# Performance work log

Measured on AMD Instinct MI355X. Metric: run time of the kernel, lower is better.

## Reference

```python
import jax, jax.numpy as jnp
import numpy as np
import math

B, S, K, H, NH = 4, 1024, 512, 1024, 16
HD = H // NH  # 64


def _split_heads(x):
    # [B, L, H] -> [B, NH, L, HD]
    b, l, _ = x.shape
    return x.reshape(b, l, NH, HD).transpose(0, 2, 1, 3)


def setup_inputs() -> dict:
    key = jax.random.key(0)
    ks = jax.random.split(key, 16)
    scale = 1.0 / math.sqrt(H)
    d = {
        'hidden_states': jax.random.normal(ks[0], (B, S, H), jnp.float32),
        'encoder_hidden_states': jax.random.normal(ks[1], (B, K, H), jnp.float32),
        'attention_mask': jnp.zeros((B, 1, 1, S), jnp.float32),
        'encoder_attention_mask': jnp.zeros((B, 1, 1, K), jnp.float32),
    }
    names = ['q', 'k', 'v', 'kq', 'kk', 'kv']
    for i, n in enumerate(names):
        d[f'W{n}'] = jax.random.normal(ks[2 + i], (H, H), jnp.float32) * scale
        d[f'b{n}'] = jnp.zeros((H,), jnp.float32)
    return d


def reference(hidden_states, encoder_hidden_states, attention_mask, encoder_attention_mask,
              Wq, bq, Wk, bk, Wv, bv, Wkq, bkq, Wkk, bkk, Wkv, bkv):
    inv = 1.0 / math.sqrt(HD)
    # self branch
    q = _split_heads(hidden_states @ Wq + bq)            # [B,NH,S,HD]
    k = _split_heads(hidden_states @ Wk + bk)
    v = _split_heads(hidden_states @ Wv + bv)
    scores = jnp.einsum('bhsd,bhtd->bhst', q, k) * inv + attention_mask
    probs = jax.nn.softmax(scores, axis=-1)              # [B,NH,S,S]
    ctx = jnp.einsum('bhst,bhtd->bhsd', probs, v)
    # knowledge branch
    kq = _split_heads(hidden_states @ Wkq + bkq)          # [B,NH,S,HD]
    kk = _split_heads(encoder_hidden_states @ Wkk + bkk)  # [B,NH,K,HD]
    kv = _split_heads(encoder_hidden_states @ Wkv + bkv)
    kscores = jnp.einsum('bhsd,bhtd->bhst', kq, kk) * inv + encoder_attention_mask
    kprobs = jax.nn.softmax(kscores, axis=-1)            # [B,NH,S,K]
    kctx = jnp.einsum('bhst,bhtd->bhsd', kprobs, kv)
    # merge heads and average branches
    out = (ctx + kctx) * 0.5                             # [B,NH,S,HD]
    out = out.transpose(0, 2, 1, 3).reshape(B, S, H)
    return out
```

## Files before the change

### kernel.cpp

```cpp
#include <hip/hip_runtime.h>

#define BATCH 4
#define SEQ   1024
#define KENC  512
#define HDIM  1024
#define NHEAD 16
#define HD    64
#define LOG2E 1.44269504088896340736f

typedef __attribute__((ext_vector_type(8))) short bf16x8;
typedef __attribute__((ext_vector_type(4))) float f32x4;
typedef __attribute__((ext_vector_type(16))) float f32x16;
typedef __attribute__((ext_vector_type(4))) float f4v;
typedef __attribute__((ext_vector_type(4))) short s4v;

__device__ __forceinline__ short f2bf(float f) {
  unsigned u = __float_as_uint(f);
  u += 0x7fffu + ((u >> 16) & 1u);
  return (short)(u >> 16);
}

__device__ __forceinline__ void gload_lds16(const void* g, void* l) {
  __builtin_amdgcn_global_load_lds(
      (const __attribute__((address_space(1))) void*)g,
      (__attribute__((address_space(3))) void*)l, 16, 0, 0);
}

__device__ __forceinline__ float tmax16(const f32x16& v) {
  float a0 = fmaxf(v[0], v[1]),   a1 = fmaxf(v[2], v[3]);
  float a2 = fmaxf(v[4], v[5]),   a3 = fmaxf(v[6], v[7]);
  float a4 = fmaxf(v[8], v[9]),   a5 = fmaxf(v[10], v[11]);
  float a6 = fmaxf(v[12], v[13]), a7 = fmaxf(v[14], v[15]);
  float b0 = fmaxf(a0, a1), b1 = fmaxf(a2, a3);
  float b2 = fmaxf(a4, a5), b3 = fmaxf(a6, a7);
  return fmaxf(fmaxf(b0, b1), fmaxf(b2, b3));
}
__device__ __forceinline__ float tsum16(const f32x16& v) {
  float a0 = v[0] + v[1],   a1 = v[2] + v[3];
  float a2 = v[4] + v[5],   a3 = v[6] + v[7];
  float a4 = v[8] + v[9],   a5 = v[10] + v[11];
  float a6 = v[12] + v[13], a7 = v[14] + v[15];
  float b0 = a0 + a1, b1 = a2 + a3, b2 = a4 + a5, b3 = a6 + a7;
  return (b0 + b1) + (b2 + b3);
}

#define MF(A, B, C) __builtin_amdgcn_mfma_f32_16x16x32_bf16((A), (B), (C), 0, 0, 0)

struct PrepArgs { const float* W[6]; };

__global__ __launch_bounds__(256) void prep(PrepArgs a, short* __restrict__ wt,
                                            const float* __restrict__ hid,
                                            short* __restrict__ hbf, int n4h,
                                            const float* __restrict__ enc,
                                            short* __restrict__ ebf, int n4e) {
  __shared__ float t[32][33];
  int blk = blockIdx.x;
  if (blk < 6144) {
    int j = blk >> 10;
    int r = blk & 1023;
    int cb = (r & 31) * 32, rb = (r >> 5) * 32;
    const float* W = a.W[j];
    short* dst = wt + (size_t)j * (HDIM * HDIM);
    int tx = threadIdx.x & 31, ty = threadIdx.x >> 5;
#pragma unroll
    for (int rr = 0; rr < 4; ++rr)
      t[ty + rr * 8][tx] = W[(size_t)(rb + ty + rr * 8) * HDIM + cb + tx];
    __syncthreads();
#pragma unroll
    for (int rr = 0; rr < 4; ++rr)
      dst[(size_t)(cb + ty + rr * 8) * HDIM + rb + tx] = f2bf(t[tx][ty + rr * 8]);
  } else {
    int i = (blk - 6144) * 256 + threadIdx.x;
    const float* s;
    short* d;
    int j;
    if (i < n4h) { s = hid; d = hbf; j = i; }
    else { j = i - n4h; if (j >= n4e) return; s = enc; d = ebf; }
    f4v v = ((const f4v*)s)[j];
    s4v o;
#pragma unroll
    for (int k = 0; k < 4; ++k) o[k] = f2bf(v[k]);
    ((s4v*)d)[j] = o;
  }
}

struct ProjArgs {
  const short* X[6];
  const short* Wt[6];
  const float* bias[6];
  short* out[6];
  int M[6];
  int tshift[6];
  int mode[6];
  float scale[6];
};

__global__ __launch_bounds__(256) void proj_gemm(ProjArgs a) {
  int job = blockIdx.z;
  int M = a.M[job];
  int by = blockIdx.y;
  if (by * 128 >= M) return;
  int bx = blockIdx.x;
  const short* X = a.X[job];
  const short* W = a.Wt[job];

  __shared__ __align__(16) char Lds[65536];

  int tid = threadIdx.x, lane = tid & 63, wave = tid >> 6;
  int wr = wave >> 1, wc = wave & 1;
  int l15 = lane & 15, g4 = lane >> 4;

  f32x4 acc[4][4];
#pragma unroll
  for (int m = 0; m < 4; ++m)
#pragma unroll
    for (int n = 0; n < 4; ++n)
#pragma unroll
      for (int r = 0; r < 4; ++r) acc[m][n][r] = 0.0f;

  int arow = by * 128, brow = bx * 128;
  const int crow = lane >> 2;
  const int sgrp = (lane & 3) ^ ((lane >> 2) & 3) ^ (lane >> 4);
  const int rsw = (lane & 3) ^ (l15 >> 2);

  const char* Xb = (const char*)X;
  const char* Wb = (const char*)W;
  const size_t sac0 = ((size_t)(arow + 32 * wave + crow) * HDIM + sgrp * 8) * 2;
  const size_t sac1 = sac0 + (size_t)16 * HDIM * 2;
  const size_t sbc0 = ((size_t)(brow + 32 * wave + crow) * HDIM + sgrp * 8) * 2;
  const size_t sbc1 = sbc0 + (size_t)16 * HDIM * 2;
  const int ldA0 = wave * 2048, ldA1 = ldA0 + 1024;
  const int ldB0 = 8192 + ldA0, ldB1 = ldB0 + 1024;

  const int aoff = wr * 4096 + l15 * 64 + ((g4 ^ rsw) << 4);
  const int boff = 8192 + wc * 4096 + l15 * 64 + ((g4 ^ rsw) << 4);

#define STG_A(SBO, SKT)                                                  \
  do {                                                                   \
    gload_lds16(Xb + sac0 + (size_t)(SKT) * 64, Lds + (SBO) + ldA0);     \
    gload_lds16(Xb + sac1 + (size_t)(SKT) * 64, Lds + (SBO) + ldA1);     \
  } while (0)
#define STG_B(SBO, SKT)                                                  \
  do {                                                                   \
    gload_lds16(Wb + sbc0 + (size_t)(SKT) * 64, Lds + (SBO) + ldB0);     \
    gload_lds16(Wb + sbc1 + (size_t)(SKT) * 64, Lds + (SBO) + ldB1);     \
  } while (0)

  STG_A(0, 0);     STG_B(0, 0);
  STG_A(16384, 1); STG_B(16384, 1);
  STG_A(32768, 2); STG_B(32768, 2);
  asm volatile("s_waitcnt vmcnt(4)" ::: "memory");
  __builtin_amdgcn_s_barrier();
  asm volatile("" ::: "memory");

  bf16x8 xa0, xa1, xb0, xb1, xb2, xb3;
  bf16x8 ya0, ya1, yb0, yb1, yb2, yb3;

  xa0 = *(const bf16x8*)(Lds + 0 * 1024 + aoff);
  xa1 = *(const bf16x8*)(Lds + 1 * 1024 + aoff);
  xb0 = *(const bf16x8*)(Lds + 0 * 1024 + boff);
  xb1 = *(const bf16x8*)(Lds + 1 * 1024 + boff);
  xb2 = *(const bf16x8*)(Lds + 2 * 1024 + boff);
  xb3 = *(const bf16x8*)(Lds + 3 * 1024 + boff);

#define GSTEP_I(BO, BON, CA0, CA1, CB0, CB1, CB2, CB3, NA0, NA1, NB0, NB1,    \
                NB2, NB3, DO_STG, SBO, SKT, DO_NEXT, VMASM, DO_BAR)           \
  do {                                                                        \
    bf16x8 q2 = *(const bf16x8*)(Lds + (BO) + 2 * 1024 + aoff);               \
    bf16x8 q3 = *(const bf16x8*)(Lds + (BO) + 3 * 1024 + aoff);               \
    if (DO_STG) STG_A(SBO, SKT);                                              \
    __builtin_amdgcn_s_setprio(1);                                            \
    acc[0][0] = MF(CA0, CB0, acc[0][0]);                                      \
    acc[0][1] = MF(CA0, CB1, acc[0][1]);                                      \
    acc[0][2] = MF(CA0, CB2, acc[0][2]);                                      \
    acc[0][3] = MF(CA0, CB3, acc[0][3]);                                      \
    acc[1][0] = MF(CA1, CB0, acc[1][0]);                                      \
    acc[1][1] = MF(CA1, CB1, acc[1][1]);                                      \
    acc[1][2] = MF(CA1, CB2, acc[1][2]);                                      \
    acc[1][3] = MF(CA1, CB3, acc[1][3]);                                      \
    __builtin_amdgcn_s_setprio(0);                                            \
    if (DO_NEXT) {                                                            \
      NA0 = *(const bf16x8*)(Lds + (BON) + 0 * 1024 + aoff);                  \
      NA1 = *(const bf16x8*)(Lds + (BON) + 1 * 1024 + aoff);                  \
      NB0 = *(const bf16x8*)(Lds + (BON) + 0 * 1024 + boff);                  \
      NB1 = *(const bf16x8*)(Lds + (BON) + 1 * 1024 + boff);                  \
      NB2 = *(const bf16x8*)(Lds + (BON) + 2 * 1024 + boff);                  \
      NB3 = *(const bf16x8*)(Lds + (BON) + 3 * 1024 + boff);                  \
    }                                                                         \
    if (DO_STG) STG_B(SBO, SKT);                                              \
    __builtin_amdgcn_s_setprio(1);                                            \
    acc[2][0] = MF(q2, CB0, acc[2][0]);                                       \
    acc[2][1] = MF(q2, CB1, acc[2][1]);                                       \
    acc[2][2] = MF(q2, CB2, acc[2][2]);                                       \
    acc[2][3] = MF(q2, CB3, acc[2][3]);                                       \
    acc[3][0] = MF(q3, CB0, acc[3][0]);                                       \
    acc[3][1] = MF(q3, CB1, acc[3][1]);                                       \
    acc[3][2] = MF(q3, CB2, acc[3][2]);                                       \
    acc[3][3] = MF(q3, CB3, acc[3][3]);                                       \
    __builtin_amdgcn_s_setprio(0);                                            \
    asm volatile(VMASM ::: "memory");                                         \
    if (DO_BAR) {                                                             \
      __builtin_amdgcn_s_barrier();                                           \
      asm volatile("" ::: "memory");                                          \
    }                                                                         \
  } while (0)
#define GSTEP(...) GSTEP_I(__VA_ARGS__)

#define XSET xa0, xa1, xb0, xb1, xb2, xb3
#define YSET ya0, ya1, yb0, yb1, yb2, yb3

#pragma unroll 1
  for (int it = 0; it < 7; ++it) {
    int t0 = it * 4;
    GSTEP(0,     16384, XSET, YSET, 1, 49152, t0 + 3, 1, "s_waitcnt vmcnt(4)", 1);
    GSTEP(16384, 32768, YSET, XSET, 1, 0,     t0 + 4, 1, "s_waitcnt vmcnt(4)", 1);
    GSTEP(32768, 49152, XSET, YSET, 1, 16384, t0 + 5, 1, "s_waitcnt vmcnt(4)", 1);
    GSTEP(49152, 0,     YSET, XSET, 1, 32768, t0 + 6, 1, "s_waitcnt vmcnt(4)", 1);
  }
  GSTEP(0,     16384, XSET, YSET, 1, 49152, 31, 1, "s_waitcnt vmcnt(4)", 1);
  GSTEP(16384, 32768, YSET, XSET, 0, 0, 0,      1, "s_waitcnt vmcnt(0)", 1);
  GSTEP(32768, 49152, XSET, YSET, 0, 0, 0,      1, "s_nop 0", 1);
  GSTEP(49152, 0,     YSET, XSET, 0, 0, 0,      0, "s_nop 0", 0);

#undef GSTEP
#undef GSTEP_I
#undef XSET
#undef YSET
#undef STG_A
#undef STG_B

  const float* bias = a.bias[job];
  short* out = a.out[job];
  int tshift = a.tshift[job], tmask = (1 << tshift) - 1, mode = a.mode[job];
  float scl = a.scale[job];
#pragma unroll
  for (int m = 0; m < 4; ++m) {
    int rowb = arow + wr * 64 + m * 16 + (g4 << 2);
#pragma unroll
    for (int n = 0; n < 4; ++n) {
      int col = brow + wc * 64 + n * 16 + l15;
      float bv = bias[col];
      int head = col >> 6, d = col & 63;
#pragma unroll
      for (int r = 0; r < 4; ++r) {
        int row = rowb + r;
        int bb = row >> tshift, tk = row & tmask;
        float val = (acc[m][n][r] + bv) * scl;
        size_t idx;
        if (mode == 0)
          idx = ((((size_t)bb * NHEAD + head) << tshift) + tk) * 64 + d;
        else
          idx = ((((size_t)bb * NHEAD + head) * 64 + d) << tshift) + tk;
        out[idx] = f2bf(val);
      }
    }
  }
}

__global__ __launch_bounds__(128, 2) void attn32(
    const short* __restrict__ qall, const short* __restrict__ kall,
    const short* __restrict__ vTall, const short* __restrict__ kqall,
    const short* __restrict__ kkall, const short* __restrict__ kvTall,
    const float* __restrict__ amask, const float* __restrict__ emask,
    float* __restrict__ out) {
  __shared__ char KT[2][8192];
  __shared__ char VT[2][8192];
  __shared__ float red[2][32];

  int lid = blockIdx.x;
  int id = (lid & 7) * 128 + (lid >> 3);
  int bh = id >> 4, qb = id & 15;
  int b = bh >> 4, h = bh & 15;
  int lane = threadIdx.x & 63, wave = threadIdx.x >> 6;
  int l31 = lane & 31, hi = lane >> 5, x7 = l31 & 7;
  int qrow0 = qb * 64 + wave * 32;

  bf16x8 qcur[4];
  {
    const short* qp = qall + ((size_t)bh * SEQ + qrow0 + l31) * 64;
#pragma unroll
    for (int i = 0; i < 4; ++i)
      qcur[i] = *(const bf16x8*)(qp + i * 16 + hi * 8);
  }

  const char* kb0 = (const char*)(kall + (size_t)bh * SEQ * 64);
  const char* vb0 = (const char*)(vTall + (size_t)bh * 64 * SEQ);
  const char* kb1 = (const char*)(kkall + (size_t)bh * KENC * 64);
  const char* vb1 = (const char*)(kvTall + (size_t)bh * 64 * KENC);
  const float* mpc = amask + (size_t)b * SEQ;

  auto STAGE = [&](int pb, const char* kb, const char* vb, size_t vrowb, int kt) {
    int t0 = threadIdx.x;
#pragma unroll
    for (int c = 0; c < 4; ++c) {
      int idx = c * 128 + t0;
      int row = idx >> 3, phys = idx & 7;
      int lg = phys ^ (row & 7);
      gload_lds16(kb + ((size_t)(kt * 64 + row)) * 128 + lg * 16,
                  KT[pb] + idx * 16);
      gload_lds16(vb + (size_t)row * vrowb + (size_t)kt * 128 + lg * 16,
                  VT[pb] + idx * 16);
    }
  };

  STAGE(0, kb0, vb0, SEQ * 2, 0);

  f32x16 ctx0, ctx1, c10, c11;
#pragma unroll
  for (int r = 0; r < 16; ++r) { ctx0[r] = 0.f; ctx1[r] = 0.f; c10[r] = 0.f; c11[r] = 0.f; }
  float mr = -1e30f, lr = 0.f;

#pragma unroll 1
  for (int t = 0; t < 24; ++t) {
    int p = t & 1;
    __syncthreads();
    if (t < 23) {
      int tn = t + 1;
      if (tn >= 16) STAGE(p ^ 1, kb1, vb1, KENC * 2, tn - 16);
      else          STAGE(p ^ 1, kb0, vb0, SEQ * 2, tn);
    }
    if (t == 16) {
      if (!hi) red[wave][l31] = lr;
      asm volatile("s_waitcnt lgkmcnt(0)" ::: "memory");
#pragma unroll
      for (int r2 = 0; r2 < 4; ++r2) {
        f4v lv = *(const f4v*)(&red[wave][r2 * 8 + 4 * hi]);
#pragma unroll
        for (int j2 = 0; j2 < 4; ++j2) {
          float li = __builtin_amdgcn_rcpf(lv[j2]);
          int r = r2 * 4 + j2;
          c10[r] = ctx0[r] * li;  ctx0[r] = 0.f;
          c11[r] = ctx1[r] * li;  ctx1[r] = 0.f;
        }
      }
      mr = -1e30f; lr = 0.f;
      const short* kqp = kqall + ((size_t)bh * SEQ + qrow0 + l31) * 64;
#pragma unroll
      for (int i = 0; i < 4; ++i)
        qcur[i] = *(const bf16x8*)(kqp + i * 16 + hi * 8);
      mpc = emask + (size_t)b * KENC;
    }
    int kt = (t >= 16) ? t - 16 : t;
    const char* Kp = KT[p];
    const char* Vp = VT[p];

    f32x16 s0, s1;
#pragma unroll
    for (int r = 0; r < 16; ++r) { s0[r] = 0.f; s1[r] = 0.f; }
    __builtin_amdgcn_s_setprio(1);
#pragma unroll
    for (int i = 0; i < 4; ++i) {
      bf16x8 kf = *(const bf16x8*)(Kp + (l31)*128 + (((2 * i + hi) ^ x7) << 4));
      s0 = __builtin_amdgcn_mfma_f32_32x32x16_bf16(kf, qcur[i], s0, 0, 0, 0);
    }
#pragma unroll
    for (int i = 0; i < 4; ++i) {
      bf16x8 kf = *(const bf16x8*)(Kp + (32 + l31) * 128 + (((2 * i + hi) ^ x7) << 4));
      s1 = __builtin_amdgcn_mfma_f32_32x32x16_bf16(kf, qcur[i], s1, 0, 0, 0);
    }
    __builtin_amdgcn_s_setprio(0);

    const float* mp = mpc + kt * 64;
#pragma unroll
    for (int r2 = 0; r2 < 4; ++r2) {
      f4v ma = *(const f4v*)(mp + r2 * 8 + 4 * hi);
      f4v mb = *(const f4v*)(mp + 32 + r2 * 8 + 4 * hi);
#pragma unroll
      for (int j2 = 0; j2 < 4; ++j2) {
        s0[r2 * 4 + j2] = fmaf(ma[j2], LOG2E, s0[r2 * 4 + j2]);
        s1[r2 * 4 + j2] = fmaf(mb[j2], LOG2E, s1[r2 * 4 + j2]);
      }
    }

    float mx = fmaxf(tmax16(s0), tmax16(s1));
    mx = fmaxf(mx, __int_as_float(__shfl_xor(__float_as_int(mx), 32)));

    if (!__all(mx <= mr + 12.f)) {
      float mn = fmaxf(mr, mx);
      float scl = __builtin_amdgcn_exp2f(mr - mn);
      mr = mn; lr *= scl;
      if (!hi) red[wave][l31] = scl;
      asm volatile("s_waitcnt lgkmcnt(0)" ::: "memory");
#pragma unroll
      for (int r2 = 0; r2 < 4; ++r2) {
        f4v sv = *(const f4v*)(&red[wave][r2 * 8 + 4 * hi]);
#pragma unroll
        for (int j2 = 0; j2 < 4; ++j2) {
          ctx0[r2 * 4 + j2] *= sv[j2];
          ctx1[r2 * 4 + j2] *= sv[j2];
        }
      }
    }

#pragma unroll
    for (int r = 0; r < 16; ++r) s0[r] = __builtin_amdgcn_exp2f(s0[r] - mr);
#pragma unroll
    for (int r = 0; r < 16; ++r) s1[r] = __builtin_amdgcn_exp2f(s1[r] - mr);
    float rs = tsum16(s0) + tsum16(s1);
    rs += __int_as_float(__shfl_xor(__float_as_int(rs), 32));
    lr += rs;

#pragma unroll
    for (int s = 0; s < 2; ++s) {
      const f32x16& sv = s ? s1 : s0;
      unsigned W[8];
#pragma unroll
      for (int r2 = 0; r2 < 4; ++r2) {
        asm("v_cvt_pk_bf16_f32 %0, %1, %2"
            : "=v"(W[r2 * 2]) : "v"(sv[r2 * 4 + 0]), "v"(sv[r2 * 4 + 1]));
        asm("v_cvt_pk_bf16_f32 %0, %1, %2"
            : "=v"(W[r2 * 2 + 1]) : "v"(sv[r2 * 4 + 2]), "v"(sv[r2 * 4 + 3]));
      }
#pragma unroll
      for (int jr = 0; jr < 2; ++jr) {
        unsigned sendA = hi ? W[(2 * jr) * 2]     : W[(2 * jr + 1) * 2];
        unsigned sendB = hi ? W[(2 * jr) * 2 + 1] : W[(2 * jr + 1) * 2 + 1];
        unsigned rA = (unsigned)__shfl_xor((int)sendA, 32);
        unsigned rB = (unsigned)__shfl_xor((int)sendB, 32);
        union { unsigned u[4]; bf16x8 v; } pa;
        if (!hi) { pa.u[0] = W[2 * jr * 2]; pa.u[1] = W[2 * jr * 2 + 1];
                   pa.u[2] = rA;            pa.u[3] = rB; }
        else     { pa.u[0] = rA;            pa.u[1] = rB;
                   pa.u[2] = W[(2 * jr + 1) * 2]; pa.u[3] = W[(2 * jr + 1) * 2 + 1]; }
        int j = s * 2 + jr;
        __builtin_amdgcn_s_setprio(1);
        bf16x8 vf0 = *(const bf16x8*)(Vp + (l31)*128 + (((2 * j + hi) ^ x7) << 4));
        ctx0 = __builtin_amdgcn_mfma_f32_32x32x16_bf16(pa.v, vf0, ctx0, 0, 0, 0);
        bf16x8 vf1 = *(const bf16x8*)(Vp + (32 + l31) * 128 + (((2 * j + hi) ^ x7) << 4));
        ctx1 = __builtin_amdgcn_mfma_f32_32x32x16_bf16(pa.v, vf1, ctx1, 0, 0, 0);
        __builtin_amdgcn_s_setprio(0);
      }
    }
  }

  if (!hi) red[wave][l31] = lr;
  asm volatile("s_waitcnt lgkmcnt(0)" ::: "memory");
  float* op = out + ((size_t)b * SEQ) * HDIM + h * 64 + l31;
#pragma unroll
  for (int r2 = 0; r2 < 4; ++r2) {
    f4v lv = *(const f4v*)(&red[wave][r2 * 8 + 4 * hi]);
#pragma unroll
    for (int j2 = 0; j2 < 4; ++j2) {
      float li = __builtin_amdgcn_rcpf(lv[j2]);
      int s = qrow0 + r2 * 8 + 4 * hi + j2;
      int r = r2 * 4 + j2;
      op[(size_t)s * HDIM]      = 0.5f * (c10[r] + ctx0[r] * li);
      op[(size_t)s * HDIM + 32] = 0.5f * (c11[r] + ctx1[r] * li);
    }
  }
}

extern "C" void kernel_launch(void* const* d_in, const int* in_sizes, int n_in,
                              void* d_out, int out_size, void* d_ws, size_t ws_size,
                              hipStream_t stream) {
  const float* hid = (const float*)d_in[0];
  const float* enc = (const float*)d_in[1];
  const float* amask = (const float*)d_in[2];
  const float* emask = (const float*)d_in[3];

  char* ws = (char*)d_ws;
  short* hbf = (short*)(ws);
  short* ebf = (short*)(ws + (8u << 20));
  short* wt = (short*)(ws + (12u << 20));
  short* qo = (short*)(ws + (24u << 20));
  short* ko = (short*)(ws + (32u << 20));
  short* vT = (short*)(ws + (40u << 20));
  short* kqo = (short*)(ws + (48u << 20));
  short* kko = (short*)(ws + (56u << 20));
  short* kvT = (short*)(ws + (60u << 20));

  PrepArgs wa;
  for (int j = 0; j < 6; ++j) wa.W[j] = (const float*)d_in[4 + 2 * j];
  prep<<<12288, 256, 0, stream>>>(wa, wt, hid, hbf, (BATCH * SEQ * HDIM) / 4,
                                  enc, ebf, (BATCH * KENC * HDIM) / 4);

  ProjArgs pa;
  const short* Xs[6] = {hbf, hbf, hbf, hbf, ebf, ebf};
  short* outs[6] = {qo, ko, vT, kqo, kko, kvT};
  const int Ms[6] = {4096, 4096, 4096, 4096, 2048, 2048};
  const int tsh[6] = {10, 10, 10, 10, 9, 9};
  const int md[6] = {0, 0, 1, 0, 0, 1};
  const float qscale = 0.125f * LOG2E;
  const float scl[6] = {qscale, 1.f, 1.f, qscale, 1.f, 1.f};
  for (int j = 0; j < 6; ++j) {
    pa.X[j] = Xs[j];
    pa.Wt[j] = wt + (size_t)j * (HDIM * HDIM);
    pa.bias[j] = (const float*)d_in[5 + 2 * j];
    pa.out[j] = outs[j];
    pa.M[j] = Ms[j];
    pa.tshift[j] = tsh[j];
    pa.mode[j] = md[j];
    pa.scale[j] = scl[j];
  }
  proj_gemm<<<dim3(8, 32, 6), 256, 0, stream>>>(pa);

  attn32<<<1024, 128, 0, stream>>>(qo, ko, vT, kqo, kko, kvT, amask, emask,
                                   (float*)d_out);
}
```

Baseline: 139.7 us.

## Rewrite projection GEMM with 256x256 tiles, 8 waves, and compact job grid

Replaces the 128x128-tile, 4-wave projection GEMM with a 256x256-tile, 8-wave kernel. It uses 128KB of LDS, 64-wide K slices with double buffering, and a new XOR swizzle. The 3D grid with early-exit blocks becomes a flat 320-block grid that maps block ids directly to job and tile, so no empty blocks launch. Larger tiles raise operand reuse and cut global traffic. The cost is fewer blocks (320 on a GPU with 256 CUs, leaving an unbalanced tail), more barriers per phase, and higher register pressure from 128 accumulators per thread.

Measured after the change: 162.9 us. +16.5%, slower.

```diff
diff --git a/kernel.cpp b/kernel.cpp
--- a/kernel.cpp
+++ b/kernel.cpp
@@ -89,156 +89,141 @@
   const short* Wt[6];
   const float* bias[6];
   short* out[6];
-  int M[6];
   int tshift[6];
   int mode[6];
   float scale[6];
 };
 
-__global__ __launch_bounds__(256) void proj_gemm(ProjArgs a) {
-  int job = blockIdx.z;
-  int M = a.M[job];
-  int by = blockIdx.y;
-  if (by * 128 >= M) return;
-  int bx = blockIdx.x;
-  const short* X = a.X[job];
-  const short* W = a.Wt[job];
-
-  __shared__ __align__(16) char Lds[65536];
+__global__ __launch_bounds__(512) void proj_gemm8(ProjArgs a) {
+  int id = blockIdx.x;
+  int job, bm, bn;
+  if (id < 256) { job = id >> 6; int r = id & 63; bm = r >> 2; bn = r & 3; }
+  else { int u = id - 256; job = 4 + (u >> 5); int r = u & 31; bm = r >> 2; bn = r & 3; }
+
+  const char* Xb = (const char*)a.X[job];
+  const char* Wb = (const char*)a.Wt[job];
+
+  __shared__ __align__(16) char Lds[131072];
 
   int tid = threadIdx.x, lane = tid & 63, wave = tid >> 6;
-  int wr = wave >> 1, wc = wave & 1;
-  int l15 = lane & 15, g4 = lane >> 4;
-
-  f32x4 acc[4][4];
-#pragma unroll
-  for (int m = 0; m < 4; ++m)
+  int wr = wave >> 2, wc = wave & 3;
+  int l15 = lane & 15, g4 = lane >> 4, x7 = l15 & 7;
+
+  f32x4 acc[8][4];
+#pragma unroll
+  for (int m = 0; m < 8; ++m)
 #pragma unroll
     for (int n = 0; n < 4; ++n)
 #pragma unroll
       for (int r = 0; r < 4; ++r) acc[m][n][r] = 0.0f;
 
-  int arow = by * 128, brow = bx * 128;
-  const int crow = lane >> 2;
-  const int sgrp = (lane & 3) ^ ((lane >> 2) & 3) ^ (lane >> 4);
-  const int rsw = (lane & 3) ^ (l15 >> 2);
-
-  const char* Xb = (const char*)X;
-  const char* Wb = (const char*)W;
-  const size_t sac0 = ((size_t)(arow + 32 * wave + crow) * HDIM + sgrp * 8) * 2;
-  const size_t sac1 = sac0 + (size_t)16 * HDIM * 2;
-  const size_t sbc0 = ((size_t)(brow + 32 * wave + crow) * HDIM + sgrp * 8) * 2;
-  const size_t sbc1 = sbc0 + (size_t)16 * HDIM * 2;
-  const int ldA0 = wave * 2048, ldA1 = ldA0 + 1024;
-  const int ldB0 = 8192 + ldA0, ldB1 = ldB0 + 1024;
-
-  const int aoff = wr * 4096 + l15 * 64 + ((g4 ^ rsw) << 4);
-  const int boff = 8192 + wc * 4096 + l15 * 64 + ((g4 ^ rsw) << 4);
-
-#define STG_A(SBO, SKT)                                                  \
-  do {                                                                   \
-    gload_lds16(Xb + sac0 + (size_t)(SKT) * 64, Lds + (SBO) + ldA0);     \
-    gload_lds16(Xb + sac1 + (size_t)(SKT) * 64, Lds + (SBO) + ldA1);     \
+  const int scol = (((lane & 7) ^ (lane >> 3)) << 4);
+  const size_t sA = ((size_t)(bm * 256 + wave * 8 + (lane >> 3))) * 2048 + scol;
+  const size_t sB = ((size_t)(bn * 256 + wave * 8 + (lane >> 3))) * 2048 + scol;
+  const int woff = wave * 1024;
+
+#define STG_T(SRC, SOFF, DB, KT)                                              \
+  do {                                                                        \
+    gload_lds16((SRC) + (SOFF) + (size_t)(KT) * 128, Lds + (DB) + woff);      \
+    gload_lds16((SRC) + (SOFF) + 131072 + (size_t)(KT) * 128,                 \
+                Lds + (DB) + 8192 + woff);                                    \
+    gload_lds16((SRC) + (SOFF) + 262144 + (size_t)(KT) * 128,                 \
+                Lds + (DB) + 16384 + woff);                                   \
+    gload_lds16((SRC) + (SOFF) + 393216 + (size_t)(KT) * 128,                 \
+                Lds + (DB) + 24576 + woff);                                   \
   } while (0)
-#define STG_B(SBO, SKT)                                                  \
-  do {                                                                   \
-    gload_lds16(Wb + sbc0 + (size_t)(SKT) * 64, Lds + (SBO) + ldB0);     \
-    gload_lds16(Wb + sbc1 + (size_t)(SKT) * 64, Lds + (SBO) + ldB1);     \
+#define STG_AB(SLOT, KT)                                                      \
+  do {                                                                        \
+    STG_T(Xb, sA, (SLOT) * 32768, KT);                                        \
+    STG_T(Wb, sB, 65536 + (SLOT) * 32768, KT);                                \
   } while (0)
 
-  STG_A(0, 0);     STG_B(0, 0);
-  STG_A(16384, 1); STG_B(16384, 1);
-  STG_A(32768, 2); STG_B(32768, 2);
-  asm volatile("s_waitcnt vmcnt(4)" ::: "memory");
-  __builtin_amdgcn_s_barrier();
-  asm volatile("" ::: "memory");
-
-  bf16x8 xa0, xa1, xb0, xb1, xb2, xb3;
-  bf16x8 ya0, ya1, yb0, yb1, yb2, yb3;
-
-  xa0 = *(const bf16x8*)(Lds + 0 * 1024 + aoff);
-  xa1 = *(const bf16x8*)(Lds + 1 * 1024 + aoff);
-  xb0 = *(const bf16x8*)(Lds + 0 * 1024 + boff);
-  xb1 = *(const bf16x8*)(Lds + 1 * 1024 + boff);
-  xb2 = *(const bf16x8*)(Lds + 2 * 1024 + boff);
-  xb3 = *(const bf16x8*)(Lds + 3 * 1024 + boff);
-
-#define GSTEP_I(BO, BON, CA0, CA1, CB0, CB1, CB2, CB3, NA0, NA1, NB0, NB1,    \
-                NB2, NB3, DO_STG, SBO, SKT, DO_NEXT, VMASM, DO_BAR)           \
+  const int aRow = l15 * 128;
+  const int sw0 = ((g4) ^ x7) << 4;
+  const int sw1 = ((4 + g4) ^ x7) << 4;
+  const char* apk0 = Lds + wr * 16384 + aRow + sw0;
+  const char* apk1 = Lds + wr * 16384 + aRow + sw1;
+  const char* bpk0 = Lds + 65536 + (wc >> 1) * 16384 + (wc & 1) * 8192 + aRow + sw0;
+  const char* bpk1 = Lds + 65536 + (wc >> 1) * 16384 + (wc & 1) * 8192 + aRow + sw1;
+
+  bf16x8 a0, a1, a2, a3, b0, b1, b2, b3;
+
+#define PHASE(APK, BPK, SLO, MH, DO_B, MI0)                                   \
   do {                                                                        \
-    bf16x8 q2 = *(const bf16x8*)(Lds + (BO) + 2 * 1024 + aoff);               \
-    bf16x8 q3 = *(const bf16x8*)(Lds + (BO) + 3 * 1024 + aoff);               \
-    if (DO_STG) STG_A(SBO, SKT);                                              \
+    if (DO_B) {                                                               \
+      b0 = *(const bf16x8*)((APK != APK ? (const char*)0 : (BPK)) + (SLO));   \
+      b1 = *(const bf16x8*)((BPK) + (SLO) + 2048);                            \
+      b2 = *(const bf16x8*)((BPK) + (SLO) + 4096);                            \
+      b3 = *(const bf16x8*)((BPK) + (SLO) + 6144);                            \
+    }                                                                         \
+    a0 = *(const bf16x8*)((APK) + (SLO) + (MH) * 8192);                       \
+    a1 = *(const bf16x8*)((APK) + (SLO) + (MH) * 8192 + 2048);                \
+    a2 = *(const bf16x8*)((APK) + (SLO) + (MH) * 8192 + 4096);                \
+    a3 = *(const bf16x8*)((APK) + (SLO) + (MH) * 8192 + 6144);                \
+    __builtin_amdgcn_sched_barrier(0);                                        \
+    __builtin_amdgcn_s_barrier();                                             \
+    asm volatile("s_waitcnt lgkmcnt(0)" ::: "memory");                        \
+    __builtin_amdgcn_sched_barrier(0);                                        \
     __builtin_amdgcn_s_setprio(1);                                            \
-    acc[0][0] = MF(CA0, CB0, acc[0][0]);                                      \
-    acc[0][1] = MF(CA0, CB1, acc[0][1]);                                      \
-    acc[0][2] = MF(CA0, CB2, acc[0][2]);                                      \
-    acc[0][3] = MF(CA0, CB3, acc[0][3]);                                      \
-    acc[1][0] = MF(CA1, CB0, acc[1][0]);                                      \
-    acc[1][1] = MF(CA1, CB1, acc[1][1]);                                      \
-    acc[1][2] = MF(CA1, CB2, acc[1][2]);                                      \
-    acc[1][3] = MF(CA1, CB3, acc[1][3]);                                      \
+    acc[(MI0)+0][0] = MF(a0, b0, acc[(MI0)+0][0]);                            \
+    acc[(MI0)+0][1] = MF(a0, b1, acc[(MI0)+0][1]);                            \
+    acc[(MI0)+0][2] = MF(a0, b2, acc[(MI0)+0][2]);                            \
+    acc[(MI0)+0][3] = MF(a0, b3, acc[(MI0)+0][3]);                            \
+    acc[(MI0)+1][0] = MF(a1, b0, acc[(MI0)+1][0]);                            \
+    acc[(MI0)+1][1] = MF(a1, b1, acc[(MI0)+1][1]);                            \
+    acc[(MI0)+1][2] = MF(a1, b2, acc[(MI0)+1][2]);                            \
+    acc[(MI0)+1][3] = MF(a1, b3, acc[(MI0)+1][3]);                            \
+    acc[(MI0)+2][0] = MF(a2, b0, acc[(MI0)+2][0]);                            \
+    acc[(MI0)+2][1] = MF(a2, b1, acc[(MI0)+2][1]);                            \
+    acc[(MI0)+2][2] = MF(a2, b2, acc[(MI0)+2][2]);                            \
+    acc[(MI0)+2][3] = MF(a2, b3, acc[(MI0)+2][3]);                            \
+    acc[(MI0)+3][0] = MF(a3, b0, acc[(MI0)+3][0]);                            \
+    acc[(MI0)+3][1] = MF(a3, b1, acc[(MI0)+3][1]);                            \
+    acc[(MI0)+3][2] = MF(a3, b2, acc[(MI0)+3][2]);                            \
+    acc[(MI0)+3][3] = MF(a3, b3, acc[(MI0)+3][3]);                            \
     __builtin_amdgcn_s_setprio(0);                                            \
-    if (DO_NEXT) {                                                            \
-      NA0 = *(const bf16x8*)(Lds + (BON) + 0 * 1024 + aoff);                  \
-      NA1 = *(const bf16x8*)(Lds + (BON) + 1 * 1024 + aoff);                  \
-      NB0 = *(const bf16x8*)(Lds + (BON) + 0 * 1024 + boff);                  \
-      NB1 = *(const bf16x8*)(Lds + (BON) + 1 * 1024 + boff);                  \
-      NB2 = *(const bf16x8*)(Lds + (BON) + 2 * 1024 + boff);                  \
-      NB3 = *(const bf16x8*)(Lds + (BON) + 3 * 1024 + boff);                  \
-    }                                                                         \
-    if (DO_STG) STG_B(SBO, SKT);                                              \
-    __builtin_amdgcn_s_setprio(1);                                            \
-    acc[2][0] = MF(q2, CB0, acc[2][0]);                                       \
-    acc[2][1] = MF(q2, CB1, acc[2][1]);                                       \
-    acc[2][2] = MF(q2, CB2, acc[2][2]);                                       \
-    acc[2][3] = MF(q2, CB3, acc[2][3]);                                       \
-    acc[3][0] = MF(q3, CB0, acc[3][0]);                                       \
-    acc[3][1] = MF(q3, CB1, acc[3][1]);                                       \
-    acc[3][2] = MF(q3, CB2, acc[3][2]);                                       \
-    acc[3][3] = MF(q3, CB3, acc[3][3]);                                       \
-    __builtin_amdgcn_s_setprio(0);                                            \
-    asm volatile(VMASM ::: "memory");                                         \
-    if (DO_BAR) {                                                             \
-      __builtin_amdgcn_s_barrier();                                           \
-      asm volatile("" ::: "memory");                                          \
-    }                                                                         \
+    __builtin_amdgcn_sched_barrier(0);                                        \
+    __builtin_amdgcn_s_barrier();                                             \
+    asm volatile("" ::: "memory");                                            \
   } while (0)
-#define GSTEP(...) GSTEP_I(__VA_ARGS__)
-
-#define XSET xa0, xa1, xb0, xb1, xb2, xb3
-#define YSET ya0, ya1, yb0, yb1, yb2, yb3
+
+#define GROUP(SL, NSL, KTN, DO_STG, VMSTR)                                    \
+  do {                                                                        \
+    if (DO_STG) STG_AB(NSL, KTN);                                             \
+    asm volatile(VMSTR ::: "memory");                                         \
+    __builtin_amdgcn_s_barrier();                                             \
+    asm volatile("" ::: "memory");                                            \
+    PHASE(apk0, bpk0, (SL) * 32768, 0, 1, 0);                                 \
+    PHASE(apk0, bpk0, (SL) * 32768, 1, 0, 4);                                 \
+    PHASE(apk1, bpk1, (SL) * 32768, 0, 1, 0);                                 \
+    PHASE(apk1, bpk1, (SL) * 32768, 1, 0, 4);                                 \
+  } while (0)
+
+  STG_AB(0, 0);
 
 #pragma unroll 1
-  for (int it = 0; it < 7; ++it) {
-    int t0 = it * 4;
-    GSTEP(0,     16384, XSET, YSET, 1, 49152, t0 + 3, 1, "s_waitcnt vmcnt(4)", 1);
-    GSTEP(16384, 32768, YSET, XSET, 1, 0,     t0 + 4, 1, "s_waitcnt vmcnt(4)", 1);
-    GSTEP(32768, 49152, XSET, YSET, 1, 16384, t0 + 5, 1, "s_waitcnt vmcnt(4)", 1);
-    GSTEP(49152, 0,     YSET, XSET, 1, 32768, t0 + 6, 1, "s_waitcnt vmcnt(4)", 1);
-  }
-  GSTEP(0,     16384, XSET, YSET, 1, 49152, 31, 1, "s_waitcnt vmcnt(4)", 1);
-  GSTEP(16384, 32768, YSET, XSET, 0, 0, 0,      1, "s_waitcnt vmcnt(0)", 1);
-  GSTEP(32768, 49152, XSET, YSET, 0, 0, 0,      1, "s_nop 0", 1);
-  GSTEP(49152, 0,     YSET, XSET, 0, 0, 0,      0, "s_nop 0", 0);
-
-#undef GSTEP
-#undef GSTEP_I
-#undef XSET
-#undef YSET
-#undef STG_A
-#undef STG_B
+  for (int h = 0; h < 14; h += 2) {
+    GROUP(0, 1, h + 1, 1, "s_waitcnt vmcnt(8)");
+    GROUP(1, 0, h + 2, 1, "s_waitcnt vmcnt(8)");
+  }
+  GROUP(0, 1, 15, 1, "s_waitcnt vmcnt(8)");
+  GROUP(1, 0, 0, 0, "s_waitcnt vmcnt(0)");
+
+#undef GROUP
+#undef PHASE
+#undef STG_AB
+#undef STG_T
 
   const float* bias = a.bias[job];
   short* out = a.out[job];
   int tshift = a.tshift[job], tmask = (1 << tshift) - 1, mode = a.mode[job];
   float scl = a.scale[job];
 #pragma unroll
-  for (int m = 0; m < 4; ++m) {
-    int rowb = arow + wr * 64 + m * 16 + (g4 << 2);
+  for (int m = 0; m < 8; ++m) {
+    int rowb = bm * 256 + wr * 128 + m * 16 + (g4 << 2);
 #pragma unroll
     for (int n = 0; n < 4; ++n) {
-      int col = brow + wc * 64 + n * 16 + l15;
+      int col = bn * 256 + wc * 64 + n * 16 + l15;
       float bv = bias[col];
       int head = col >> 6, d = col & 63;
 #pragma unroll
@@ -477,7 +462,6 @@
   ProjArgs pa;
   const short* Xs[6] = {hbf, hbf, hbf, hbf, ebf, ebf};
   short* outs[6] = {qo, ko, vT, kqo, kko, kvT};
-  const int Ms[6] = {4096, 4096, 4096, 4096, 2048, 2048};
   const int tsh[6] = {10, 10, 10, 10, 9, 9};
   const int md[6] = {0, 0, 1, 0, 0, 1};
   const float qscale = 0.125f * LOG2E;
@@ -487,12 +471,11 @@
     pa.Wt[j] = wt + (size_t)j * (HDIM * HDIM);
     pa.bias[j] = (const float*)d_in[5 + 2 * j];
     pa.out[j] = outs[j];
-    pa.M[j] = Ms[j];
     pa.tshift[j] = tsh[j];
     pa.mode[j] = md[j];
     pa.scale[j] = scl[j];
   }
-  proj_gemm<<<dim3(8, 32, 6), 256, 0, stream>>>(pa);
+  proj_gemm8<<<320, 512, 0, stream>>>(pa);
 
   attn32<<<1024, 128, 0, stream>>>(qo, ko, vT, kqo, kko, kvT, amask, emask,
                                    (float*)d_out);
```

## Use K=64 tiles with double buffering in projection GEMM

Applied to the files above, without the earlier changes.

Restructures the projection GEMM main loop from 32-wide K tiles in a 4-stage LDS ring to 64-wide K tiles in a 2-stage double buffer, with a new XOR swizzle on 128-byte rows. Each step now does two half-tile fragment loads and 32 MFMAs per wave, cutting the number of barriers and loop steps in half. The cost is less prefetch depth: each step waits for all outstanding loads (vmcnt(0)), so global load latency may be less well hidden than with the deeper pipeline.

Measured after the change: 142.7 us. 2.1% more time.

```diff
diff --git a/kernel.cpp b/kernel.cpp
--- a/kernel.cpp
+++ b/kernel.cpp
@@ -108,7 +108,7 @@
 
   int tid = threadIdx.x, lane = tid & 63, wave = tid >> 6;
   int wr = wave >> 1, wc = wave & 1;
-  int l15 = lane & 15, g4 = lane >> 4;
+  int l15 = lane & 15, g4 = lane >> 4, x7 = l15 & 7;
 
   f32x4 acc[4][4];
 #pragma unroll
@@ -119,113 +119,103 @@
       for (int r = 0; r < 4; ++r) acc[m][n][r] = 0.0f;
 
   int arow = by * 128, brow = bx * 128;
-  const int crow = lane >> 2;
-  const int sgrp = (lane & 3) ^ ((lane >> 2) & 3) ^ (lane >> 4);
-  const int rsw = (lane & 3) ^ (l15 >> 2);
-
+
+  const int srow = lane >> 3;
+  const int scol = (((lane & 7) ^ srow) << 4);
   const char* Xb = (const char*)X;
   const char* Wb = (const char*)W;
-  const size_t sac0 = ((size_t)(arow + 32 * wave + crow) * HDIM + sgrp * 8) * 2;
-  const size_t sac1 = sac0 + (size_t)16 * HDIM * 2;
-  const size_t sbc0 = ((size_t)(brow + 32 * wave + crow) * HDIM + sgrp * 8) * 2;
-  const size_t sbc1 = sbc0 + (size_t)16 * HDIM * 2;
-  const int ldA0 = wave * 2048, ldA1 = ldA0 + 1024;
-  const int ldB0 = 8192 + ldA0, ldB1 = ldB0 + 1024;
-
-  const int aoff = wr * 4096 + l15 * 64 + ((g4 ^ rsw) << 4);
-  const int boff = 8192 + wc * 4096 + l15 * 64 + ((g4 ^ rsw) << 4);
-
-#define STG_A(SBO, SKT)                                                  \
-  do {                                                                   \
-    gload_lds16(Xb + sac0 + (size_t)(SKT) * 64, Lds + (SBO) + ldA0);     \
-    gload_lds16(Xb + sac1 + (size_t)(SKT) * 64, Lds + (SBO) + ldA1);     \
+  const size_t sA = ((size_t)(arow + wave * 32 + srow)) * 2048 + scol;
+  const size_t sB = ((size_t)(brow + wave * 32 + srow)) * 2048 + scol;
+  const int woff = wave * 4096;
+
+#define STG_A(BUF, KT)                                                        \
+  do {                                                                        \
+    gload_lds16(Xb + sA + (size_t)(KT) * 128,          Lds + (BUF) + woff);   \
+    gload_lds16(Xb + sA + (size_t)(KT) * 128 + 16384,  Lds + (BUF) + woff + 1024); \
+    gload_lds16(Xb + sA + (size_t)(KT) * 128 + 32768,  Lds + (BUF) + woff + 2048); \
+    gload_lds16(Xb + sA + (size_t)(KT) * 128 + 49152,  Lds + (BUF) + woff + 3072); \
   } while (0)
-#define STG_B(SBO, SKT)                                                  \
-  do {                                                                   \
-    gload_lds16(Wb + sbc0 + (size_t)(SKT) * 64, Lds + (SBO) + ldB0);     \
-    gload_lds16(Wb + sbc1 + (size_t)(SKT) * 64, Lds + (SBO) + ldB1);     \
+#define STG_B(BUF, KT)                                                        \
+  do {                                                                        \
+    gload_lds16(Wb + sB + (size_t)(KT) * 128,          Lds + (BUF) + 16384 + woff); \
+    gload_lds16(Wb + sB + (size_t)(KT) * 128 + 16384,  Lds + (BUF) + 16384 + woff + 1024); \
+    gload_lds16(Wb + sB + (size_t)(KT) * 128 + 32768,  Lds + (BUF) + 16384 + woff + 2048); \
+    gload_lds16(Wb + sB + (size_t)(KT) * 128 + 49152,  Lds + (BUF) + 16384 + woff + 3072); \
   } while (0)
 
-  STG_A(0, 0);     STG_B(0, 0);
-  STG_A(16384, 1); STG_B(16384, 1);
-  STG_A(32768, 2); STG_B(32768, 2);
-  asm volatile("s_waitcnt vmcnt(4)" ::: "memory");
+  const int sw0 = (g4 ^ x7) << 4;
+  const int aoff = (wr * 64 + l15) * 128 + sw0;
+  const int boff = 16384 + (wc * 64 + l15) * 128 + sw0;
+
+  STG_A(0, 0);
+  STG_B(0, 0);
+  asm volatile("s_waitcnt vmcnt(0)" ::: "memory");
   __builtin_amdgcn_s_barrier();
   asm volatile("" ::: "memory");
 
-  bf16x8 xa0, xa1, xb0, xb1, xb2, xb3;
-  bf16x8 ya0, ya1, yb0, yb1, yb2, yb3;
-
-  xa0 = *(const bf16x8*)(Lds + 0 * 1024 + aoff);
-  xa1 = *(const bf16x8*)(Lds + 1 * 1024 + aoff);
-  xb0 = *(const bf16x8*)(Lds + 0 * 1024 + boff);
-  xb1 = *(const bf16x8*)(Lds + 1 * 1024 + boff);
-  xb2 = *(const bf16x8*)(Lds + 2 * 1024 + boff);
-  xb3 = *(const bf16x8*)(Lds + 3 * 1024 + boff);
-
-#define GSTEP_I(BO, BON, CA0, CA1, CB0, CB1, CB2, CB3, NA0, NA1, NB0, NB1,    \
-                NB2, NB3, DO_STG, SBO, SKT, DO_NEXT, VMASM, DO_BAR)           \
+#define HALF(BO, KH, A0, A1, A2, A3, B0, B1, B2, B3)                          \
   do {                                                                        \
-    bf16x8 q2 = *(const bf16x8*)(Lds + (BO) + 2 * 1024 + aoff);               \
-    bf16x8 q3 = *(const bf16x8*)(Lds + (BO) + 3 * 1024 + aoff);               \
-    if (DO_STG) STG_A(SBO, SKT);                                              \
+    A0 = *(const bf16x8*)(Lds + (BO) + 0 * 2048 + (aoff ^ ((KH) * 0x40)));    \
+    A1 = *(const bf16x8*)(Lds + (BO) + 1 * 2048 + (aoff ^ ((KH) * 0x40)));    \
+    A2 = *(const bf16x8*)(Lds + (BO) + 2 * 2048 + (aoff ^ ((KH) * 0x40)));    \
+    A3 = *(const bf16x8*)(Lds + (BO) + 3 * 2048 + (aoff ^ ((KH) * 0x40)));    \
+    B0 = *(const bf16x8*)(Lds + (BO) + 0 * 2048 + (boff ^ ((KH) * 0x40)));    \
+    B1 = *(const bf16x8*)(Lds + (BO) + 1 * 2048 + (boff ^ ((KH) * 0x40)));    \
+    B2 = *(const bf16x8*)(Lds + (BO) + 2 * 2048 + (boff ^ ((KH) * 0x40)));    \
+    B3 = *(const bf16x8*)(Lds + (BO) + 3 * 2048 + (boff ^ ((KH) * 0x40)));    \
+  } while (0)
+
+#define MM16(A0, A1, A2, A3, B0, B1, B2, B3)                                  \
+  do {                                                                        \
     __builtin_amdgcn_s_setprio(1);                                            \
-    acc[0][0] = MF(CA0, CB0, acc[0][0]);                                      \
-    acc[0][1] = MF(CA0, CB1, acc[0][1]);                                      \
-    acc[0][2] = MF(CA0, CB2, acc[0][2]);                                      \
-    acc[0][3] = MF(CA0, CB3, acc[0][3]);                                      \
-    acc[1][0] = MF(CA1, CB0, acc[1][0]);                                      \
-    acc[1][1] = MF(CA1, CB1, acc[1][1]);                                      \
-    acc[1][2] = MF(CA1, CB2, acc[1][2]);                                      \
-    acc[1][3] = MF(CA1, CB3, acc[1][3]);                                      \
+    acc[0][0] = MF(A0, B0, acc[0][0]);                                        \
+    acc[0][1] = MF(A0, B1, acc[0][1]);                                        \
+    acc[0][2] = MF(A0, B2, acc[0][2]);                                        \
+    acc[0][3] = MF(A0, B3, acc[0][3]);                                        \
+    acc[1][0] = MF(A1, B0, acc[1][0]);                                        \
+    acc[1][1] = MF(A1, B1, acc[1][1]);                                        \
+    acc[1][2] = MF(A1, B2, acc[1][2]);                                        \
+    acc[1][3] = MF(A1, B3, acc[1][3]);                                        \
+    acc[2][0] = MF(A2, B0, acc[2][0]);                                        \
+    acc[2][1] = MF(A2, B1, acc[2][1]);                                        \
+    acc[2][2] = MF(A2, B2, acc[2][2]);                                        \
+    acc[2][3] = MF(A2, B3, acc[2][3]);                                        \
+    acc[3][0] = MF(A3, B0, acc[3][0]);                                        \
+    acc[3][1] = MF(A3, B1, acc[3][1]);                                        \
+    acc[3][2] = MF(A3, B2, acc[3][2]);                                        \
+    acc[3][3] = MF(A3, B3, acc[3][3]);                                        \
     __builtin_amdgcn_s_setprio(0);                                            \
-    if (DO_NEXT) {                                                            \
-      NA0 = *(const bf16x8*)(Lds + (BON) + 0 * 1024 + aoff);                  \
-      NA1 = *(const bf16x8*)(Lds + (BON) + 1 * 1024 + aoff);                  \
-      NB0 = *(const bf16x8*)(Lds + (BON) + 0 * 1024 + boff);                  \
-      NB1 = *(const bf16x8*)(Lds + (BON) + 1 * 1024 + boff);                  \
-      NB2 = *(const bf16x8*)(Lds + (BON) + 2 * 1024 + boff);                  \
-      NB3 = *(const bf16x8*)(Lds + (BON) + 3 * 1024 + boff);                  \
-    }                                                                         \
-    if (DO_STG) STG_B(SBO, SKT);                                              \
-    __builtin_amdgcn_s_setprio(1);                                            \
-    acc[2][0] = MF(q2, CB0, acc[2][0]);                                       \
-    acc[2][1] = MF(q2, CB1, acc[2][1]);                                       \
-    acc[2][2] = MF(q2, CB2, acc[2][2]);                                       \
-    acc[2][3] = MF(q2, CB3, acc[2][3]);                                       \
-    acc[3][0] = MF(q3, CB0, acc[3][0]);                                       \
-    acc[3][1] = MF(q3, CB1, acc[3][1]);                                       \
-    acc[3][2] = MF(q3, CB2, acc[3][2]);                                       \
-    acc[3][3] = MF(q3, CB3, acc[3][3]);                                       \
-    __builtin_amdgcn_s_setprio(0);                                            \
-    asm volatile(VMASM ::: "memory");                                         \
+  } while (0)
+
+#define STEP(BO, OB, KTN, DO_STG, VMW, DO_BAR)                                \
+  do {                                                                        \
+    bf16x8 pa0, pa1, pa2, pa3, pb0, pb1, pb2, pb3;                            \
+    bf16x8 qa0, qa1, qa2, qa3, qb0, qb1, qb2, qb3;                            \
+    HALF(BO, 0, pa0, pa1, pa2, pa3, pb0, pb1, pb2, pb3);                      \
+    if (DO_STG) STG_A(OB, KTN);                                               \
+    MM16(pa0, pa1, pa2, pa3, pb0, pb1, pb2, pb3);                             \
+    HALF(BO, 1, qa0, qa1, qa2, qa3, qb0, qb1, qb2, qb3);                      \
+    if (DO_STG) STG_B(OB, KTN);                                               \
+    MM16(qa0, qa1, qa2, qa3, qb0, qb1, qb2, qb3);                             \
+    asm volatile(VMW ::: "memory");                                           \
     if (DO_BAR) {                                                             \
       __builtin_amdgcn_s_barrier();                                           \
       asm volatile("" ::: "memory");                                          \
     }                                                                         \
   } while (0)
-#define GSTEP(...) GSTEP_I(__VA_ARGS__)
-
-#define XSET xa0, xa1, xb0, xb1, xb2, xb3
-#define YSET ya0, ya1, yb0, yb1, yb2, yb3
 
 #pragma unroll 1
   for (int it = 0; it < 7; ++it) {
-    int t0 = it * 4;
-    GSTEP(0,     16384, XSET, YSET, 1, 49152, t0 + 3, 1, "s_waitcnt vmcnt(4)", 1);
-    GSTEP(16384, 32768, YSET, XSET, 1, 0,     t0 + 4, 1, "s_waitcnt vmcnt(4)", 1);
-    GSTEP(32768, 49152, XSET, YSET, 1, 16384, t0 + 5, 1, "s_waitcnt vmcnt(4)", 1);
-    GSTEP(49152, 0,     YSET, XSET, 1, 32768, t0 + 6, 1, "s_waitcnt vmcnt(4)", 1);
-  }
-  GSTEP(0,     16384, XSET, YSET, 1, 49152, 31, 1, "s_waitcnt vmcnt(4)", 1);
-  GSTEP(16384, 32768, YSET, XSET, 0, 0, 0,      1, "s_waitcnt vmcnt(0)", 1);
-  GSTEP(32768, 49152, XSET, YSET, 0, 0, 0,      1, "s_nop 0", 1);
-  GSTEP(49152, 0,     YSET, XSET, 0, 0, 0,      0, "s_nop 0", 0);
-
-#undef GSTEP
-#undef GSTEP_I
-#undef XSET
-#undef YSET
+    int t0 = it * 2;
+    STEP(0,     32768, t0 + 1, 1, "s_waitcnt vmcnt(0)", 1);
+    STEP(32768, 0,     t0 + 2, 1, "s_waitcnt vmcnt(0)", 1);
+  }
+  STEP(0,     32768, 15, 1, "s_waitcnt vmcnt(0)", 1);
+  STEP(32768, 0,     0,  0, "s_nop 0", 0);
+
+#undef STEP
+#undef MM16
+#undef HALF
 #undef STG_A
 #undef STG_B
 
```
